# Performance work log

Hardware: AMD Instinct MI355X
Metric: run time of the kernel (lower is better)

Reference implementation:

```python
import jax, jax.numpy as jnp
import numpy as np

NUM_HEADS = 20
MAX_SEQLEN = 1500  # max per-segment length (Whisper 30s -> 1500 frames); static for jit
NEG = -1e30


def setup_inputs() -> dict:
    key = jax.random.key(0)
    ks = jax.random.split(key, 6)
    B, S, D = 4, MAX_SEQLEN, 1280
    T = B * S
    hidden_states = jax.random.normal(ks[0], (T, D), dtype=jnp.float32)
    # packed varlen layout: 4 equal-length audio segments
    cu_seqlens = (jnp.arange(B + 1, dtype=jnp.int32) * S)
    w = 0.02
    Wq = jax.random.normal(ks[1], (D, D), dtype=jnp.float32) * w
    Wk = jax.random.normal(ks[2], (D, D), dtype=jnp.float32) * w
    Wv = jax.random.normal(ks[3], (D, D), dtype=jnp.float32) * w
    Wo = jax.random.normal(ks[4], (D, D), dtype=jnp.float32) * w
    bq = jnp.zeros((D,), jnp.float32)
    bv = jnp.zeros((D,), jnp.float32)
    bo = jnp.zeros((D,), jnp.float32)
    return {"hidden_states": hidden_states, "cu_seqlens": cu_seqlens,
            "Wq": Wq, "bq": bq, "Wk": Wk, "Wv": Wv, "bv": bv, "Wo": Wo, "bo": bo}


def _varlen_attention(hidden_states, cu_seqlens, Wq, bq, Wk, Wv, bv, Wo, bo):
    T, D = hidden_states.shape
    H = NUM_HEADS
    d = D // H
    scale = d ** -0.5
    S = MAX_SEQLEN
    B = cu_seqlens.shape[0] - 1

    # projections (torch nn.Linear convention: y = x @ W.T + b; k_proj has no bias)
    q = hidden_states @ Wq.T + bq   # [T, D]
    k = hidden_states @ Wk.T        # [T, D]
    v = hidden_states @ Wv.T + bv   # [T, D]

    lens = cu_seqlens[1:] - cu_seqlens[:-1]                 # [B]
    pos = jnp.arange(S, dtype=jnp.int32)                    # [S]
    valid = pos[None, :] < lens[:, None]                    # [B, S]
    idx = cu_seqlens[:-1, None] + pos[None, :]              # [B, S]
    idx_g = jnp.where(valid, idx, 0)

    # unpack to padded [B, S, H, d]
    qb = q[idx_g].reshape(B, S, H, d)
    kb = k[idx_g].reshape(B, S, H, d)
    vb = v[idx_g].reshape(B, S, H, d)

    scores = jnp.einsum('bqhd,bkhd->bhqk', qb, kb) * scale  # [B, H, S, S]
    scores = jnp.where(valid[:, None, None, :], scores, NEG)
    attn = jax.nn.softmax(scores, axis=-1)
    out = jnp.einsum('bhqk,bkhd->bqhd', attn, vb).reshape(B, S, D)

    # repack to [T, D]; invalid slots scatter out-of-bounds and are dropped
    idx_s = jnp.where(valid, idx, T).reshape(-1)
    packed = jnp.zeros((T, D), out.dtype).at[idx_s].set(out.reshape(-1, D), mode='drop')
    return packed @ Wo.T + bo


def reference(hidden_states, cu_seqlens, Wq, bq, Wk, Wv, bv, Wo, bo):
    return _varlen_attention(hidden_states, cu_seqlens, Wq, bq, Wk, Wv, bv, Wo, bo)
```

## Files before the change

kernel.cpp:

```cpp
#include <hip/hip_runtime.h>
#include <stdint.h>
#include <math.h>

#define DMODEL 1280
#define NHEAD  20
#define DHEAD  64
#define NSEG   4
#define MAXS   1500
#define SPAD   1536
#define TPAD   (NSEG*SPAD)
#define QT256  ((MAXS + 255) / 256)
#define BM 128
#define BN 128
#define BK 32
#define OBM 64
#define OBN 128
#define QSCALE 0.18033688011112042f
#define NEGV  -1e30f

typedef float  f32x4  __attribute__((ext_vector_type(4)));
typedef __bf16 bf16x8 __attribute__((ext_vector_type(8)));

#if __has_builtin(__builtin_amdgcn_exp2f)
#define EXP2F(x) __builtin_amdgcn_exp2f(x)
#else
#define EXP2F(x) exp2f(x)
#endif

__device__ __forceinline__ ushort f2bf(float f) {
  union { float f; uint32_t u; } a; a.f = f;
  uint32_t u = a.u;
  u += 0x7FFFu + ((u >> 16) & 1u);
  return (ushort)(u >> 16);
}

__device__ __forceinline__ void async16(const void* g, void* lds) {
  __builtin_amdgcn_global_load_lds((const __attribute__((address_space(1))) void*)g,
                                   (__attribute__((address_space(3))) void*)lds,
                                   16, 0, 0);
}

__device__ __forceinline__ int perm32(int a) {
  return ((a >> 2) & 3) * 8 + ((a >> 4) & 1) * 4 + (a & 3);
}

__global__ void __launch_bounds__(256)
cvt_all(const float* __restrict__ hs, const float* __restrict__ Wq,
        const float* __restrict__ Wk, const float* __restrict__ Wv,
        const float* __restrict__ Wo, ushort* __restrict__ dst, int nX, int DD) {
  const int ng = (nX + 4 * DD) >> 3;
  const int stride = gridDim.x * 256;
  for (int g = blockIdx.x * 256 + threadIdx.x; g < ng; g += stride) {
    const int i = g << 3;
    const float* src;
    if (i < nX) {
      src = hs + i;
    } else {
      const int j = i - nX;
      const int z = (j >= DD) + (j >= 2 * DD) + (j >= 3 * DD);
      const float* w = (z == 0) ? Wq : (z == 1) ? Wk : (z == 2) ? Wv : Wo;
      src = w + (j - z * DD);
    }
    const float4 v0 = ((const float4*)src)[0];
    const float4 v1 = ((const float4*)src)[1];
    ushort4 o0, o1;
    o0.x = f2bf(v0.x); o0.y = f2bf(v0.y); o0.z = f2bf(v0.z); o0.w = f2bf(v0.w);
    o1.x = f2bf(v1.x); o1.y = f2bf(v1.y); o1.z = f2bf(v1.z); o1.w = f2bf(v1.w);
    ((ushort4*)(dst + i))[0] = o0;
    ((ushort4*)(dst + i))[1] = o1;
  }
}

__device__ __forceinline__ void gemm_tile_mainloop(
    const ushort* __restrict__ A, const ushort* __restrict__ W,
    int M, int m0, int n0, ushort* As, ushort* Bs, f32x4 (&acc)[4][4])
{
  const int tid  = threadIdx.x;
  const int wave = tid >> 6, lane = tid & 63;
  const int quad = lane >> 4, c16 = lane & 15;
  const int wr = (wave >> 1) * 64, wc = (wave & 1) * 64;

  const int M0 = wave * 128 + lane, M1 = M0 + 64;
  const int sr0 = M0 >> 3, pp0 = M0 & 7, p0 = pp0 ^ (sr0 & 7);
  const int sr1 = M1 >> 3, pp1 = M1 & 7, p1 = pp1 ^ (sr1 & 7);
  const int row0 = sr0 * 2 + (p0 >> 2), kc0 = (p0 & 3) << 3;
  const int row1 = sr1 * 2 + (p1 >> 2), kc1 = (p1 & 3) << 3;
  const ushort* Ap0 = A + (size_t)(m0 + row0) * DMODEL + kc0;
  const ushort* Ap1 = A + (size_t)(m0 + row1) * DMODEL + kc1;
  const ushort* Bp0 = W + (size_t)(n0 + row0) * DMODEL + kc0;
  const ushort* Bp1 = W + (size_t)(n0 + row1) * DMODEL + kc1;
  const int o0 = wave * 1024;
  const int o1 = wave * 1024 + 512;
  const int BUF = BM * BK;

  async16(Ap0, As + o0); async16(Ap1, As + o1);
  async16(Bp0, Bs + o0); async16(Bp1, Bs + o1);

  int c = 0;
  for (int k0 = 0; k0 < DMODEL; k0 += BK, c ^= 1) {
    __syncthreads();
    if (k0 + BK < DMODEL) {
      const int kn = k0 + BK;
      const int bo = (c ^ 1) * BUF;
      async16(Ap0 + kn, As + bo + o0); async16(Ap1 + kn, As + bo + o1);
      async16(Bp0 + kn, Bs + bo + o0); async16(Bp1 + kn, Bs + bo + o1);
    }
    const ushort* Ab = As + c * BUF;
    const ushort* Bb = Bs + c * BUF;
    bf16x8 a[4], b[4];
#pragma unroll
    for (int i = 0; i < 4; ++i) {
      const int row = wr + i * 16 + c16;
      const int sr = row >> 1;
      const int off = (sr << 6) + (((((row & 1) << 2) | quad) ^ (sr & 7)) << 3);
      a[i] = *(const bf16x8*)(Ab + off);
    }
#pragma unroll
    for (int j = 0; j < 4; ++j) {
      const int row = wc + j * 16 + c16;
      const int sr = row >> 1;
      const int off = (sr << 6) + (((((row & 1) << 2) | quad) ^ (sr & 7)) << 3);
      b[j] = *(const bf16x8*)(Bb + off);
    }
#pragma unroll
    for (int i = 0; i < 4; ++i)
#pragma unroll
      for (int j = 0; j < 4; ++j)
        acc[i][j] = __builtin_amdgcn_mfma_f32_16x16x32_bf16(a[i], b[j], acc[i][j], 0, 0, 0);
  }
}

__global__ void __launch_bounds__(256, 4)
gemm_qkv(const ushort* __restrict__ X, const ushort* __restrict__ W4,
         const float* __restrict__ bq, const float* __restrict__ bv,
         const int* __restrict__ cu,
         ushort* __restrict__ qb, ushort* __restrict__ kb, ushort* __restrict__ vt, int M)
{
  __shared__ ushort As[2 * BM * BK], Bs[2 * BN * BK];
  const int wg = blockIdx.x;
  if (wg >= 30) return;
  const int z = wg / 10;
  const int n0 = (wg % 10) * BN;
  const int m0 = blockIdx.y * BM;
  const ushort* W = W4 + (size_t)z * DMODEL * DMODEL;

  f32x4 acc[4][4];
  f32x4 zero = {0.f, 0.f, 0.f, 0.f};
#pragma unroll
  for (int i = 0; i < 4; ++i)
#pragma unroll
    for (int j = 0; j < 4; ++j) acc[i][j] = zero;

  gemm_tile_mainloop(X, W, M, m0, n0, As, Bs, acc);

  const int tid = threadIdx.x, wave = tid >> 6, lane = tid & 63;
  const int quad = lane >> 4, c16 = lane & 15;
  const int wr = (wave >> 1) * 64, wc = (wave & 1) * 64;

  if (z == 2) {
    const int c1 = cu[1], c2 = cu[2], c3 = cu[3];
#pragma unroll
    for (int i = 0; i < 4; ++i) {
      const int t0 = m0 + wr + i * 16 + quad * 4;
      const int s0a = (t0 >= c1) + (t0 >= c2) + (t0 >= c3);
      const int s3a = (t0 + 3 >= c1) + (t0 + 3 >= c2) + (t0 + 3 >= c3);
      const int seg0 = (s0a == 0) ? 0 : (s0a == 1) ? c1 : (s0a == 2) ? c2 : c3;
#pragma unroll
      for (int j = 0; j < 4; ++j) {
        const int cfeat = n0 + wc + j * 16 + c16;
        const float bb = bv[cfeat];
        if (t0 + 3 < M && s0a == s3a) {
          const int s = t0 - seg0;
          const size_t base = (size_t)cfeat * TPAD + (size_t)s0a * SPAD
                            + (size_t)(s & ~31) + perm32(s & 31);
          ushort4 w;
          w.x = f2bf(acc[i][j][0] + bb);
          w.y = f2bf(acc[i][j][1] + bb);
          w.z = f2bf(acc[i][j][2] + bb);
          w.w = f2bf(acc[i][j][3] + bb);
          *(ushort4*)(vt + base) = w;
        } else {
#pragma unroll
          for (int r = 0; r < 4; ++r) {
            const int t = t0 + r;
            if (t < M) {
              const int sb = (t >= c1) + (t >= c2) + (t >= c3);
              const int sg = (sb == 0) ? 0 : (sb == 1) ? c1 : (sb == 2) ? c2 : c3;
              const int s = t - sg;
              vt[(size_t)cfeat * TPAD + (size_t)sb * SPAD + (s & ~31) + perm32(s & 31)]
                  = f2bf(acc[i][j][r] + bb);
            }
          }
        }
      }
    }
  } else {
    ushort* out = (z == 0) ? qb : kb;
    const float* bias = (z == 0) ? bq : (const float*)nullptr;
    const float oscale = (z == 0) ? QSCALE : 1.0f;
#pragma unroll
    for (int i = 0; i < 4; ++i) {
      const int rbase = m0 + wr + i * 16 + quad * 4;
#pragma unroll
      for (int j = 0; j < 4; ++j) {
        const int c = n0 + wc + j * 16 + c16;
        const float bb = bias ? bias[c] : 0.f;
#pragma unroll
        for (int r = 0; r < 4; ++r) {
          const int rr = rbase + r;
          if (rr < M) out[(size_t)rr * DMODEL + c] = f2bf((acc[i][j][r] + bb) * oscale);
        }
      }
    }
  }
}

__global__ void __launch_bounds__(128, 3)
gemm_out(const ushort* __restrict__ A, const ushort* __restrict__ W,
         const float* __restrict__ bias, float* __restrict__ out, int M)
{
  __shared__ ushort As[2 * OBM * BK], Bs[2 * OBN * BK];
  const int n0 = blockIdx.x * OBN;
  const int m0 = blockIdx.y * OBM;
  const int tid = threadIdx.x, wave = tid >> 6, lane = tid & 63;
  const int quad = lane >> 4, c16 = lane & 15;

  int rA[2], kA[2], rB[4], kB[4];
#pragma unroll
  for (int q = 0; q < 2; ++q) {
    const int s = tid + q * 128;
    const int sr = s >> 3, p = (s & 7) ^ (sr & 7);
    rA[q] = sr * 2 + (p >> 2); kA[q] = (p & 3) << 3;
  }
#pragma unroll
  for (int q = 0; q < 4; ++q) {
    const int s = tid + q * 128;
    const int sr = s >> 3, p = (s & 7) ^ (sr & 7);
    rB[q] = sr * 2 + (p >> 2); kB[q] = (p & 3) << 3;
  }
  const ushort* ApS0 = A + (size_t)(m0 + rA[0]) * DMODEL + kA[0];
  const ushort* ApS1 = A + (size_t)(m0 + rA[1]) * DMODEL + kA[1];
  const ushort* BpS0 = W + (size_t)(n0 + rB[0]) * DMODEL + kB[0];
  const ushort* BpS1 = W + (size_t)(n0 + rB[1]) * DMODEL + kB[1];
  const ushort* BpS2 = W + (size_t)(n0 + rB[2]) * DMODEL + kB[2];
  const ushort* BpS3 = W + (size_t)(n0 + rB[3]) * DMODEL + kB[3];
  const int aO0 = (wave * 64) * 8,       aO1 = (128 + wave * 64) * 8;
  const int bO0 = (wave * 64) * 8,       bO1 = (128 + wave * 64) * 8;
  const int bO2 = (256 + wave * 64) * 8, bO3 = (384 + wave * 64) * 8;
  const int BUFA = OBM * BK;
  const int BUFB = OBN * BK;

#define OSTAGE(c, kk) do { \
    ushort* Ad = As + (c) * BUFA; ushort* Bd = Bs + (c) * BUFB; \
    async16(ApS0 + (kk), Ad + aO0); async16(ApS1 + (kk), Ad + aO1); \
    async16(BpS0 + (kk), Bd + bO0); async16(BpS1 + (kk), Bd + bO1); \
    async16(BpS2 + (kk), Bd + bO2); async16(BpS3 + (kk), Bd + bO3); \
  } while (0)

  f32x4 acc[4][4];
  f32x4 zero = {0.f, 0.f, 0.f, 0.f};
#pragma unroll
  for (int i = 0; i < 4; ++i)
#pragma unroll
    for (int j = 0; j < 4; ++j) acc[i][j] = zero;

  OSTAGE(0, 0);
  int c = 0;
  for (int k0 = 0; k0 < DMODEL; k0 += BK, c ^= 1) {
    __syncthreads();
    if (k0 + BK < DMODEL) OSTAGE(c ^ 1, k0 + BK);
    const ushort* Ab = As + c * BUFA;
    const ushort* Bb = Bs + c * BUFB;
    bf16x8 a[4], b[4];
#pragma unroll
    for (int i = 0; i < 4; ++i) {
      const int row = i * 16 + c16;
      const int sr = row >> 1;
      const int off = (sr << 6) + (((((row & 1) << 2) | quad) ^ (sr & 7)) << 3);
      a[i] = *(const bf16x8*)(Ab + off);
    }
#pragma unroll
    for (int j = 0; j < 4; ++j) {
      const int row = wave * 64 + j * 16 + c16;
      const int sr = row >> 1;
      const int off = (sr << 6) + (((((row & 1) << 2) | quad) ^ (sr & 7)) << 3);
      b[j] = *(const bf16x8*)(Bb + off);
    }
#pragma unroll
    for (int i = 0; i < 4; ++i)
#pragma unroll
      for (int j = 0; j < 4; ++j)
        acc[i][j] = __builtin_amdgcn_mfma_f32_16x16x32_bf16(a[i], b[j], acc[i][j], 0, 0, 0);
  }
#undef OSTAGE

#pragma unroll
  for (int i = 0; i < 4; ++i) {
    const int rbase = m0 + i * 16 + quad * 4;
#pragma unroll
    for (int j = 0; j < 4; ++j) {
      const int cc = n0 + wave * 64 + j * 16 + c16;
      const float bb = bias[cc];
#pragma unroll
      for (int r = 0; r < 4; ++r) {
        const int rr = rbase + r;
        if (rr < M) out[(size_t)rr * DMODEL + cc] = acc[i][j][r] + bb;
      }
    }
  }
}

__global__ void __launch_bounds__(512, 4)
attn_fused(const ushort* __restrict__ qb, const ushort* __restrict__ kb,
           const ushort* __restrict__ vt, ushort* __restrict__ ob,
           const int* __restrict__ cu, int T)
{
  __shared__ ushort SB[16384];
  const int hs = blockIdx.x;
  const int b = hs / NHEAD, h = hs % NHEAD;
  const int seg0 = cu[b];
  const int len  = cu[b + 1] - seg0;
  const int q0 = blockIdx.y * 256;
  if (q0 >= len) return;
  const int tid = threadIdx.x, wave = tid >> 6, lane = tid & 63;
  const int quad = lane >> 4, c16 = lane & 15;

#pragma unroll
  for (int t = 0; t < 4; ++t) {
    const int slot = t * 512 + tid;
    const int r = slot >> 3, k2 = slot & 7;
    const int col = ((k2 ^ (r & 7)) << 3);
    async16(qb + (size_t)(seg0 + q0 + r) * DMODEL + h * DHEAD + col,
            &SB[(t * 512 + wave * 64) * 8]);
  }

  const int rK = tid >> 3, kK = tid & 7;
  const int colK = ((kK ^ (rK & 7)) << 3);
  const ushort* kp = kb + (size_t)(seg0 + rK) * DMODEL + h * DHEAD + colK;
  const ushort* vp = vt + (size_t)(h * DHEAD + rK) * TPAD + (size_t)b * SPAD + colK;
  const int ldsoff = wave * 512;

  __syncthreads();

  bf16x8 aq[2][2];
#pragma unroll
  for (int n = 0; n < 2; ++n)
#pragma unroll
    for (int ks = 0; ks < 2; ++ks) {
      const int row = wave * 32 + n * 16 + c16;
      aq[n][ks] = *(const bf16x8*)(&SB[row * 64 + (((ks * 4 + quad) ^ (c16 & 7)) << 3)]);
    }

  __syncthreads();

  async16(kp, &SB[ldsoff]); async16(vp, &SB[4096 + ldsoff]);
  kp += (size_t)64 * DMODEL; vp += 64;

  float l_i[2] = {0.f, 0.f};
  f32x4 o_acc[2][4];
  f32x4 zero = {0.f, 0.f, 0.f, 0.f};
#pragma unroll
  for (int n = 0; n < 2; ++n)
#pragma unroll
    for (int m = 0; m < 4; ++m) o_acc[n][m] = zero;

  const int niter = (len + 63) >> 6;
  for (int it = 0; it < niter; ++it) {
    __syncthreads();
    const ushort* Kt = &SB[(it & 1) * 8192];
    const ushort* Vt = Kt + 4096;

    if (it + 1 < niter) {
      ushort* Dst = &SB[((it + 1) & 1) * 8192];
      async16(kp, Dst + ldsoff); async16(vp, Dst + 4096 + ldsoff);
      kp += (size_t)64 * DMODEL; vp += 64;
    }

    f32x4 s[2][4];
    __builtin_amdgcn_s_setprio(1);
#pragma unroll
    for (int f = 0; f < 4; ++f) {
      const int row = f * 16 + c16;
      const int ch = c16 & 7;
      bf16x8 ak0 = *(const bf16x8*)(Kt + row * 64 + ((quad ^ ch) << 3));
      bf16x8 ak1 = *(const bf16x8*)(Kt + row * 64 + (((4 + quad) ^ ch) << 3));
#pragma unroll
      for (int n = 0; n < 2; ++n) {
        s[n][f] = zero;
        s[n][f] = __builtin_amdgcn_mfma_f32_16x16x32_bf16(ak0, aq[n][0], s[n][f], 0, 0, 0);
        s[n][f] = __builtin_amdgcn_mfma_f32_16x16x32_bf16(ak1, aq[n][1], s[n][f], 0, 0, 0);
      }
    }
    __builtin_amdgcn_s_setprio(0);

    const int kv0 = it * 64;
    if (kv0 + 64 > len) {
#pragma unroll
      for (int f = 0; f < 4; ++f) {
        const int kvb = kv0 + f * 16 + quad * 4;
#pragma unroll
        for (int r = 0; r < 4; ++r)
          if (kvb + r >= len) { s[0][f][r] = NEGV; s[1][f][r] = NEGV; }
      }
    }

#pragma unroll
    for (int n = 0; n < 2; ++n) {
      float rs = 0.f;
#pragma unroll
      for (int f = 0; f < 4; ++f)
#pragma unroll
        for (int r = 0; r < 4; ++r) {
          const float p = EXP2F(s[n][f][r]);
          s[n][f][r] = p;
          rs += p;
        }
      l_i[n] += rs;
    }

    bf16x8 bp[2][2];
#pragma unroll
    for (int n = 0; n < 2; ++n)
#pragma unroll
      for (int g = 0; g < 2; ++g) {
        bf16x8 t;
#pragma unroll
        for (int r = 0; r < 4; ++r) {
          t[r]     = (__bf16)s[n][2 * g][r];
          t[r + 4] = (__bf16)s[n][2 * g + 1][r];
        }
        bp[n][g] = t;
      }

    __builtin_amdgcn_s_setprio(1);
#pragma unroll
    for (int m = 0; m < 4; ++m) {
      const int row = m * 16 + c16;
      const int ch = c16 & 7;
      bf16x8 av0 = *(const bf16x8*)(Vt + row * 64 + ((quad ^ ch) << 3));
      bf16x8 av1 = *(const bf16x8*)(Vt + row * 64 + (((4 + quad) ^ ch) << 3));
#pragma unroll
      for (int n = 0; n < 2; ++n) {
        o_acc[n][m] = __builtin_amdgcn_mfma_f32_16x16x32_bf16(av0, bp[n][0], o_acc[n][m], 0, 0, 0);
        o_acc[n][m] = __builtin_amdgcn_mfma_f32_16x16x32_bf16(av1, bp[n][1], o_acc[n][m], 0, 0, 0);
      }
    }
    __builtin_amdgcn_s_setprio(0);
  }

#pragma unroll
  for (int n = 0; n < 2; ++n) {
    float l = l_i[n];
    l += __shfl_xor(l, 16);
    l += __shfl_xor(l, 32);
    const int q = q0 + wave * 32 + n * 16 + c16;
    if (q < len) {
      const float inv = 1.0f / l;
      const size_t base = (size_t)(seg0 + q) * DMODEL + h * DHEAD;
#pragma unroll
      for (int m = 0; m < 4; ++m) {
        ushort4 pk;
        pk.x = f2bf(o_acc[n][m][0] * inv);
        pk.y = f2bf(o_acc[n][m][1] * inv);
        pk.z = f2bf(o_acc[n][m][2] * inv);
        pk.w = f2bf(o_acc[n][m][3] * inv);
        *(ushort4*)(ob + base + m * 16 + quad * 4) = pk;
      }
    }
  }
}

extern "C" void kernel_launch(void* const* d_in, const int* in_sizes, int n_in,
                              void* d_out, int out_size, void* d_ws, size_t ws_size,
                              hipStream_t stream)
{
  (void)n_in; (void)out_size; (void)ws_size;
  const float* hs = (const float*)d_in[0];
  const int*   cu = (const int*)d_in[1];
  const float* Wq = (const float*)d_in[2];
  const float* bq = (const float*)d_in[3];
  const float* Wk = (const float*)d_in[4];
  const float* Wv = (const float*)d_in[5];
  const float* bv = (const float*)d_in[6];
  const float* Wo = (const float*)d_in[7];
  const float* bo = (const float*)d_in[8];
  float* out = (float*)d_out;
  const int T  = in_sizes[0] / DMODEL;
  const int DD = DMODEL * DMODEL;
  const int nX = T * DMODEL;

  ushort* ws  = (ushort*)d_ws;
  ushort* X   = ws;
  ushort* W4  = X + (size_t)nX;
  ushort* qb  = W4 + 4 * (size_t)DD;
  ushort* kb  = qb + (size_t)T * DMODEL;
  ushort* vt  = kb + (size_t)T * DMODEL;
  ushort* ob  = X;

  cvt_all<<<2048, 256, 0, stream>>>(hs, Wq, Wk, Wv, Wo, ws, nX, DD);

  gemm_qkv<<<dim3(32, (T + BM - 1) / BM), 256, 0, stream>>>(
      X, W4, bq, bv, cu, qb, kb, vt, T);

  attn_fused<<<dim3(NSEG * NHEAD, QT256), 512, 0, stream>>>(qb, kb, vt, ob, cu, T);

  gemm_out<<<dim3(10, (T + OBM - 1) / OBM), 128, 0, stream>>>(
      ob, W4 + 3 * (size_t)DD, bo, out, T);
}
```

Measured before the change: 296.6 us.

## Fuse fp32-to-bf16 conversion into QKV GEMM loads, convert only Wo separately

Removes the separate pass that converted hidden states and all four weight matrices to bf16. The QKV GEMM now reads fp32 operands straight from global memory into registers, converts them to bf16 and stores them into swizzled LDS, prefetching the next K slice in registers. Only Wo is still pre-converted, for the output GEMM. This saves a full read/write pass over X and three weights, but each GEMM tile now reads fp32 data (twice the bytes), repeated across the N tiles. It also drops the async direct-to-LDS loads and lowers occupancy to 3 blocks per CU.

```diff
diff --git a/kernel.cpp b/kernel.cpp
--- a/kernel.cpp
+++ b/kernel.cpp
@@ -44,35 +44,27 @@
   return ((a >> 2) & 3) * 8 + ((a >> 4) & 1) * 4 + (a & 3);
 }
 
+__device__ __forceinline__ bf16x8 cvt8(float4 u, float4 v) {
+  bf16x8 t;
+  t[0] = (__bf16)u.x; t[1] = (__bf16)u.y; t[2] = (__bf16)u.z; t[3] = (__bf16)u.w;
+  t[4] = (__bf16)v.x; t[5] = (__bf16)v.y; t[6] = (__bf16)v.z; t[7] = (__bf16)v.w;
+  return t;
+}
+
 __global__ void __launch_bounds__(256)
-cvt_all(const float* __restrict__ hs, const float* __restrict__ Wq,
-        const float* __restrict__ Wk, const float* __restrict__ Wv,
-        const float* __restrict__ Wo, ushort* __restrict__ dst, int nX, int DD) {
-  const int ng = (nX + 4 * DD) >> 3;
-  const int stride = gridDim.x * 256;
-  for (int g = blockIdx.x * 256 + threadIdx.x; g < ng; g += stride) {
-    const int i = g << 3;
-    const float* src;
-    if (i < nX) {
-      src = hs + i;
-    } else {
-      const int j = i - nX;
-      const int z = (j >= DD) + (j >= 2 * DD) + (j >= 3 * DD);
-      const float* w = (z == 0) ? Wq : (z == 1) ? Wk : (z == 2) ? Wv : Wo;
-      src = w + (j - z * DD);
-    }
-    const float4 v0 = ((const float4*)src)[0];
-    const float4 v1 = ((const float4*)src)[1];
-    ushort4 o0, o1;
-    o0.x = f2bf(v0.x); o0.y = f2bf(v0.y); o0.z = f2bf(v0.z); o0.w = f2bf(v0.w);
-    o1.x = f2bf(v1.x); o1.y = f2bf(v1.y); o1.z = f2bf(v1.z); o1.w = f2bf(v1.w);
-    ((ushort4*)(dst + i))[0] = o0;
-    ((ushort4*)(dst + i))[1] = o1;
-  }
-}
-
-__device__ __forceinline__ void gemm_tile_mainloop(
-    const ushort* __restrict__ A, const ushort* __restrict__ W,
+cvt_wo(const float* __restrict__ Wo, ushort* __restrict__ dst) {
+  const int i = (blockIdx.x * 256 + threadIdx.x) * 8;
+  const float4 v0 = ((const float4*)(Wo + i))[0];
+  const float4 v1 = ((const float4*)(Wo + i))[1];
+  ushort4 o0, o1;
+  o0.x = f2bf(v0.x); o0.y = f2bf(v0.y); o0.z = f2bf(v0.z); o0.w = f2bf(v0.w);
+  o1.x = f2bf(v1.x); o1.y = f2bf(v1.y); o1.z = f2bf(v1.z); o1.w = f2bf(v1.w);
+  ((ushort4*)(dst + i))[0] = o0;
+  ((ushort4*)(dst + i))[1] = o1;
+}
+
+__device__ __forceinline__ void gemm_f32_mainloop(
+    const float* __restrict__ A, const float* __restrict__ W,
     int M, int m0, int n0, ushort* As, ushort* Bs, f32x4 (&acc)[4][4])
 {
   const int tid  = threadIdx.x;
@@ -80,46 +72,52 @@
   const int quad = lane >> 4, c16 = lane & 15;
   const int wr = (wave >> 1) * 64, wc = (wave & 1) * 64;
 
-  const int M0 = wave * 128 + lane, M1 = M0 + 64;
-  const int sr0 = M0 >> 3, pp0 = M0 & 7, p0 = pp0 ^ (sr0 & 7);
-  const int sr1 = M1 >> 3, pp1 = M1 & 7, p1 = pp1 ^ (sr1 & 7);
-  const int row0 = sr0 * 2 + (p0 >> 2), kc0 = (p0 & 3) << 3;
-  const int row1 = sr1 * 2 + (p1 >> 2), kc1 = (p1 & 3) << 3;
-  const ushort* Ap0 = A + (size_t)(m0 + row0) * DMODEL + kc0;
-  const ushort* Ap1 = A + (size_t)(m0 + row1) * DMODEL + kc1;
-  const ushort* Bp0 = W + (size_t)(n0 + row0) * DMODEL + kc0;
-  const ushort* Bp1 = W + (size_t)(n0 + row1) * DMODEL + kc1;
-  const int o0 = wave * 1024;
-  const int o1 = wave * 1024 + 512;
+  const int rA = tid >> 1, hh = tid & 1;
+  const int rag = (m0 + rA < M) ? (m0 + rA) : (M - 1);
+  const float* Ap = A + (size_t)rag * DMODEL + hh * 16;
+  const float* Bp = W + (size_t)(n0 + rA) * DMODEL + hh * 16;
+  const int sr = rA >> 1;
+  const int p0 = ((rA & 1) << 2) | (hh << 1);
+  const int ofc0 = sr * 64 + ((p0 ^ (sr & 7)) << 3);
+  const int ofc1 = sr * 64 + (((p0 | 1) ^ (sr & 7)) << 3);
   const int BUF = BM * BK;
 
-  async16(Ap0, As + o0); async16(Ap1, As + o1);
-  async16(Bp0, Bs + o0); async16(Bp1, Bs + o1);
-
+  float4 xa0, xa1, xa2, xa3, xb0, xb1, xb2, xb3;
+#define LDF(k0) do { \
+    const float4* ap = (const float4*)(Ap + (k0)); \
+    const float4* bp = (const float4*)(Bp + (k0)); \
+    xa0 = ap[0]; xa1 = ap[1]; xa2 = ap[2]; xa3 = ap[3]; \
+    xb0 = bp[0]; xb1 = bp[1]; xb2 = bp[2]; xb3 = bp[3]; \
+  } while (0)
+
+  LDF(0);
   int c = 0;
   for (int k0 = 0; k0 < DMODEL; k0 += BK, c ^= 1) {
-    __syncthreads();
-    if (k0 + BK < DMODEL) {
-      const int kn = k0 + BK;
-      const int bo = (c ^ 1) * BUF;
-      async16(Ap0 + kn, As + bo + o0); async16(Ap1 + kn, As + bo + o1);
-      async16(Bp0 + kn, Bs + bo + o0); async16(Bp1 + kn, Bs + bo + o1);
-    }
+    ushort* Ad = As + c * BUF;
+    ushort* Bd = Bs + c * BUF;
+    *(bf16x8*)(Ad + ofc0) = cvt8(xa0, xa1);
+    *(bf16x8*)(Ad + ofc1) = cvt8(xa2, xa3);
+    *(bf16x8*)(Bd + ofc0) = cvt8(xb0, xb1);
+    *(bf16x8*)(Bd + ofc1) = cvt8(xb2, xb3);
+    if (k0 + BK < DMODEL) LDF(k0 + BK);
+    asm volatile("s_waitcnt lgkmcnt(0)" ::: "memory");
+    __builtin_amdgcn_s_barrier();
+    asm volatile("" ::: "memory");
     const ushort* Ab = As + c * BUF;
     const ushort* Bb = Bs + c * BUF;
     bf16x8 a[4], b[4];
 #pragma unroll
     for (int i = 0; i < 4; ++i) {
       const int row = wr + i * 16 + c16;
-      const int sr = row >> 1;
-      const int off = (sr << 6) + (((((row & 1) << 2) | quad) ^ (sr & 7)) << 3);
+      const int srr = row >> 1;
+      const int off = (srr << 6) + (((((row & 1) << 2) | quad) ^ (srr & 7)) << 3);
       a[i] = *(const bf16x8*)(Ab + off);
     }
 #pragma unroll
     for (int j = 0; j < 4; ++j) {
       const int row = wc + j * 16 + c16;
-      const int sr = row >> 1;
-      const int off = (sr << 6) + (((((row & 1) << 2) | quad) ^ (sr & 7)) << 3);
+      const int srr = row >> 1;
+      const int off = (srr << 6) + (((((row & 1) << 2) | quad) ^ (srr & 7)) << 3);
       b[j] = *(const bf16x8*)(Bb + off);
     }
 #pragma unroll
@@ -128,21 +126,23 @@
       for (int j = 0; j < 4; ++j)
         acc[i][j] = __builtin_amdgcn_mfma_f32_16x16x32_bf16(a[i], b[j], acc[i][j], 0, 0, 0);
   }
-}
-
-__global__ void __launch_bounds__(256, 4)
-gemm_qkv(const ushort* __restrict__ X, const ushort* __restrict__ W4,
+#undef LDF
+}
+
+__global__ void __launch_bounds__(256, 3)
+gemm_qkv(const float* __restrict__ X, const float* __restrict__ Wq,
+         const float* __restrict__ Wk, const float* __restrict__ Wv,
          const float* __restrict__ bq, const float* __restrict__ bv,
          const int* __restrict__ cu,
          ushort* __restrict__ qb, ushort* __restrict__ kb, ushort* __restrict__ vt, int M)
 {
-  __shared__ ushort As[2 * BM * BK], Bs[2 * BN * BK];
+  __shared__ __align__(16) ushort As[2 * BM * BK], Bs[2 * BN * BK];
   const int wg = blockIdx.x;
   if (wg >= 30) return;
   const int z = wg / 10;
   const int n0 = (wg % 10) * BN;
   const int m0 = blockIdx.y * BM;
-  const ushort* W = W4 + (size_t)z * DMODEL * DMODEL;
+  const float* W = (z == 0) ? Wq : (z == 1) ? Wk : Wv;
 
   f32x4 acc[4][4];
   f32x4 zero = {0.f, 0.f, 0.f, 0.f};
@@ -151,7 +151,7 @@
 #pragma unroll
     for (int j = 0; j < 4; ++j) acc[i][j] = zero;
 
-  gemm_tile_mainloop(X, W, M, m0, n0, As, Bs, acc);
+  gemm_f32_mainloop(X, W, M, m0, n0, As, Bs, acc);
 
   const int tid = threadIdx.x, wave = tid >> 6, lane = tid & 63;
   const int quad = lane >> 4, c16 = lane & 15;
@@ -219,7 +219,7 @@
 gemm_out(const ushort* __restrict__ A, const ushort* __restrict__ W,
          const float* __restrict__ bias, float* __restrict__ out, int M)
 {
-  __shared__ ushort As[2 * OBM * BK], Bs[2 * OBN * BK];
+  __shared__ __align__(16) ushort As[2 * OBM * BK], Bs[2 * OBN * BK];
   const int n0 = blockIdx.x * OBN;
   const int m0 = blockIdx.y * OBM;
   const int tid = threadIdx.x, wave = tid >> 6, lane = tid & 63;
@@ -487,23 +487,21 @@
   float* out = (float*)d_out;
   const int T  = in_sizes[0] / DMODEL;
   const int DD = DMODEL * DMODEL;
-  const int nX = T * DMODEL;
 
   ushort* ws  = (ushort*)d_ws;
-  ushort* X   = ws;
-  ushort* W4  = X + (size_t)nX;
-  ushort* qb  = W4 + 4 * (size_t)DD;
+  ushort* wo  = ws;
+  ushort* qb  = wo + (size_t)DD;
   ushort* kb  = qb + (size_t)T * DMODEL;
-  ushort* vt  = kb + (size_t)T * DMODEL;
-  ushort* ob  = X;
-
-  cvt_all<<<2048, 256, 0, stream>>>(hs, Wq, Wk, Wv, Wo, ws, nX, DD);
+  ushort* ob  = kb + (size_t)T * DMODEL;
+  ushort* vt  = ob + (size_t)T * DMODEL;
+
+  cvt_wo<<<DD / 8 / 256, 256, 0, stream>>>(Wo, wo);
 
   gemm_qkv<<<dim3(32, (T + BM - 1) / BM), 256, 0, stream>>>(
-      X, W4, bq, bv, cu, qb, kb, vt, T);
+      hs, Wq, Wk, Wv, bq, bv, cu, qb, kb, vt, T);
 
   attn_fused<<<dim3(NSEG * NHEAD, QT256), 512, 0, stream>>>(qb, kb, vt, ob, cu, T);
 
   gemm_out<<<dim3(10, (T + OBM - 1) / OBM), 128, 0, stream>>>(
-      ob, W4 + 3 * (size_t)DD, bo, out, T);
-}
+      ob, wo, bo, out, T);
+}
```

After: 364.1 us. +22.8%, slower.
